# Optimization experiments

Measured on AMD Instinct MI355X. Metric: run time of the kernel, lower is better.

The kernel has to match this reference:

```python
import jax, jax.numpy as jnp
import numpy as np

N_NODES = 100000
NEG_SLOPE = 0.2  # PyG GATConv default


def gat_conv(x, src, dst, W, a_src, a_dst, n_nodes):
    """One PyG-style GATConv (with self-loops already appended to src/dst).
    x: [N, Fin], W: [Fin, H*C], a_src/a_dst: [H, C]. Returns [N, H, C]."""
    H, C = a_src.shape
    h = (x @ W).reshape(-1, H, C)                      # [N, H, C]
    s_src = jnp.einsum('nhc,hc->nh', h, a_src)         # [N, H]
    s_dst = jnp.einsum('nhc,hc->nh', h, a_dst)         # [N, H]
    e = jax.nn.leaky_relu(s_src[src] + s_dst[dst], NEG_SLOPE)  # [E, H]
    # segment softmax over incoming edges of each destination node
    e_max = jax.ops.segment_max(e, dst, num_segments=n_nodes)  # [N, H]
    e_exp = jnp.exp(e - e_max[dst])
    denom = jax.ops.segment_sum(e_exp, dst, num_segments=n_nodes)
    alpha = e_exp / (denom[dst] + 1e-16)               # [E, H]
    msg = h[src] * alpha[:, :, None]                   # [E, H, C]
    return jax.ops.segment_sum(msg, dst, num_segments=n_nodes)  # [N, H, C]


def setup_inputs() -> dict:
    key = jax.random.key(0)
    ks = jax.random.split(key, 10)
    in_dim, hidden, heads, out_dim = 128, 32, 4, 32
    N, E = N_NODES, 1600000
    x = jax.random.normal(ks[0], (N, in_dim), dtype=jnp.float32)
    edge_index = jax.random.randint(ks[1], (2, E), 0, N, dtype=jnp.int64)
    s = 0.1
    return {
        'x': x,
        'edge_index': edge_index,
        'W1': s * jax.random.normal(ks[2], (in_dim, heads * hidden), dtype=jnp.float32),
        'a_src1': s * jax.random.normal(ks[3], (heads, hidden), dtype=jnp.float32),
        'a_dst1': s * jax.random.normal(ks[4], (heads, hidden), dtype=jnp.float32),
        'b1': jnp.zeros((heads * hidden,), dtype=jnp.float32),
        'W2': s * jax.random.normal(ks[5], (heads * hidden, out_dim), dtype=jnp.float32),
        'a_src2': s * jax.random.normal(ks[6], (1, out_dim), dtype=jnp.float32),
        'a_dst2': s * jax.random.normal(ks[7], (1, out_dim), dtype=jnp.float32),
        'b2': jnp.zeros((out_dim,), dtype=jnp.float32),
    }


def reference(x, edge_index, W1, a_src1, a_dst1, b1, W2, a_src2, a_dst2, b2):
    N = x.shape[0]
    loops = jnp.arange(N, dtype=edge_index.dtype)
    src = jnp.concatenate([edge_index[0], loops])  # PyG adds self-loops
    dst = jnp.concatenate([edge_index[1], loops])
    h1 = gat_conv(x, src, dst, W1, a_src1, a_dst1, N)      # [N, H, C]
    h1 = jax.nn.elu(h1.reshape(N, -1) + b1)                # concat heads + bias, elu
    h2 = gat_conv(h1, src, dst, W2, a_src2, a_dst2, N)     # [N, 1, out]
    return h2.mean(axis=1) + b2                            # concat=False -> mean over heads
```

## Files before the change

### kernel.cpp

```cpp
#include <hip/hip_runtime.h>
#include <hip/hip_bf16.h>

#define NEG 0.2f
#define BK_SHIFT 9
#define BK_CAP 9216

typedef short short8 __attribute__((ext_vector_type(8)));
typedef float f32x4 __attribute__((ext_vector_type(4)));

__device__ __forceinline__ float lrelu(float x){ return x > 0.f ? x : NEG * x; }
__device__ __forceinline__ float elu_f(float x){ return x > 0.f ? x : expm1f(x); }
__device__ __forceinline__ unsigned short f2bf(float f){
  unsigned int u = __float_as_uint(f);
  unsigned int r = u + 0x7fffu + ((u >> 16) & 1u);
  return (unsigned short)(r >> 16);
}
__device__ __forceinline__ float bf2f(unsigned short u){
  return __uint_as_float(((unsigned int)u) << 16);
}
__device__ __forceinline__ float2 bfu2(unsigned int v){
  float2 r;
  r.x = __uint_as_float(v << 16);
  r.y = __uint_as_float(v & 0xffff0000u);
  return r;
}

__global__ __launch_bounds__(512) void k_binA_packW(
    const int* __restrict__ src, const int* __restrict__ dst, int E,
    int* __restrict__ gcursor, int2* __restrict__ ebuf,
    const float* __restrict__ W, unsigned short* __restrict__ Wp, int nA){
  __shared__ int hist[256];
  __shared__ int base[256];
  int t = threadIdx.x;
  int bid = blockIdx.x;
  if (bid >= nA){
    int idx = (bid - nA) * 512 + t;
    int n = idx >> 7, k = idx & 127;
    Wp[n * 128 + k] = f2bf(W[(size_t)k * 128 + n]);
    return;
  }
  if (t < 256) hist[t] = 0;
  __syncthreads();
  int e0 = bid * 4096;
  for (int j = 0; j < 8; j++){
    int e = e0 + j * 512 + t;
    if (e < E) atomicAdd(&hist[dst[e] >> BK_SHIFT], 1);
  }
  __syncthreads();
  if (t < 256){
    int cnt = hist[t];
    if (cnt > 0) base[t] = atomicAdd(&gcursor[t], cnt);
    hist[t] = 0;
  }
  __syncthreads();
  for (int j = 0; j < 8; j++){
    int e = e0 + j * 512 + t;
    if (e < E){
      int d = dst[e]; int b = d >> BK_SHIFT;
      int loc = atomicAdd(&hist[b], 1);
      ebuf[(size_t)b * BK_CAP + base[b] + loc] = make_int2(src[e], d);
    }
  }
}

__global__ __launch_bounds__(256, 3) void k_csrC_gemm1(
    const int2* __restrict__ ebuf, const int* __restrict__ gcount,
    int* __restrict__ rowp, int* __restrict__ csr, int N, int NBK, int total,
    const float* __restrict__ x, const unsigned short* __restrict__ Wp,
    const float* __restrict__ a_src, const float* __restrict__ a_dst,
    unsigned short* __restrict__ h_bf, float* __restrict__ ss, float* __restrict__ sd){
  __shared__ __align__(16) unsigned short Wt[128 * 136];
  __shared__ __align__(16) unsigned short Xb[64 * 136];
  int t = threadIdx.x;

  if (blockIdx.x < (unsigned)NBK){
    int* hist = (int*)Wt;
    int* psum = hist + 512;
    int* bsum = psum + 256;
    int b = blockIdx.x;
    int nbase = b << BK_SHIFT;
    int cnt = gcount[b];
    const int2* eb = ebuf + (size_t)b * BK_CAP;
    hist[t] = 0; hist[t + 256] = 0;
    int bv = 0;
    {
      int nodes = 0;
      if (t < NBK){ int nb = N - (t << BK_SHIFT); nodes = nb > 512 ? 512 : nb; bv = gcount[t] + nodes; }
      bsum[t] = bv;
    }
    __syncthreads();
    for (int off = 1; off < 256; off <<= 1){
      int xv = (t >= off) ? bsum[t - off] : 0;
      __syncthreads();
      bsum[t] += xv;
      __syncthreads();
    }
    for (int i = t; i < cnt; i += 256)
      atomicAdd(&hist[eb[i].y - nbase], 1);
    __syncthreads();
    int v0 = hist[2 * t], v1 = hist[2 * t + 1];
    int ps = v0 + v1;
    psum[t] = ps;
    __syncthreads();
    for (int off = 1; off < 256; off <<= 1){
      int xv = (t >= off) ? psum[t - off] : 0;
      __syncthreads();
      psum[t] += xv;
      __syncthreads();
    }
    {
      int eo = psum[t] - ps;
      int bb = (b == 0) ? 0 : bsum[b - 1];
      int n0 = 2 * t, n1 = 2 * t + 1;
      int r0 = bb + eo + n0;
      int r1 = bb + eo + v0 + n1;
      if (nbase + n0 < N) rowp[nbase + n0] = r0;
      if (nbase + n1 < N) rowp[nbase + n1] = r1;
      hist[n0] = r0; hist[n1] = r1;
    }
    if (b == 0 && t == 0) rowp[N] = total;
    __syncthreads();
    for (int i = t; i < cnt; i += 256){
      int2 e = eb[i];
      int pos = atomicAdd(&hist[e.y - nbase], 1);
      csr[pos] = e.x;
    }
    __syncthreads();
    {
      int n0 = 2 * t, n1 = 2 * t + 1;
      if (nbase + n0 < N) csr[hist[n0]] = nbase + n0;
      if (nbase + n1 < N) csr[hist[n1]] = nbase + n1;
    }
    return;
  }

  int rb = (blockIdx.x - NBK) * 64;

  #pragma unroll
  for (int j = 0; j < 8; j++){
    int fi = j * 256 + t;
    int n = fi >> 4, ch = fi & 15;
    *(uint4*)&Wt[n * 136 + ch * 8] = *(const uint4*)&Wp[n * 128 + ch * 8];
  }
  #pragma unroll
  for (int j = 0; j < 8; j++){
    int fi = j * 256 + t;
    int row = fi >> 5, k4 = (fi & 31) * 4;
    int gr = rb + row;
    float4 v = make_float4(0.f, 0.f, 0.f, 0.f);
    if (gr < N) v = *(const float4*)&x[(size_t)gr * 128 + k4];
    uint2 pk;
    pk.x = ((unsigned)f2bf(v.y) << 16) | f2bf(v.x);
    pk.y = ((unsigned)f2bf(v.w) << 16) | f2bf(v.z);
    *(uint2*)&Xb[row * 136 + k4] = pk;
  }
  __syncthreads();

  int w = t >> 6, l = t & 63;
  int m = l & 15, quad = l >> 4;
  f32x4 acc[8];
  #pragma unroll
  for (int ct = 0; ct < 8; ct++) acc[ct] = (f32x4){0.f, 0.f, 0.f, 0.f};

  #pragma unroll
  for (int kc = 0; kc < 4; kc++){
    short8 a = *(const short8*)&Xb[(w * 16 + m) * 136 + kc * 32 + quad * 8];
    #pragma unroll
    for (int ct = 0; ct < 8; ct++){
      short8 bfr = *(const short8*)&Wt[(ct * 16 + m) * 136 + kc * 32 + quad * 8];
      acc[ct] = __builtin_amdgcn_mfma_f32_16x16x32_bf16(a, bfr, acc[ct], 0, 0, 0);
    }
  }

  float as[8], ad[8];
  #pragma unroll
  for (int ct = 0; ct < 8; ct++){ as[ct] = a_src[ct * 16 + m]; ad[ct] = a_dst[ct * 16 + m]; }

  #pragma unroll
  for (int reg = 0; reg < 4; reg++){
    int gr = rb + w * 16 + quad * 4 + reg;
    bool ok = gr < N;
    if (ok){
      #pragma unroll
      for (int ct = 0; ct < 8; ct++)
        h_bf[(size_t)gr * 128 + ct * 16 + m] = f2bf(acc[ct][reg]);
    }
    #pragma unroll
    for (int hh = 0; hh < 4; hh++){
      float pss = acc[2*hh][reg] * as[2*hh] + acc[2*hh+1][reg] * as[2*hh+1];
      float pd = acc[2*hh][reg] * ad[2*hh] + acc[2*hh+1][reg] * ad[2*hh+1];
      pss += __shfl_xor(pss, 1, 16); pss += __shfl_xor(pss, 2, 16);
      pss += __shfl_xor(pss, 4, 16); pss += __shfl_xor(pss, 8, 16);
      pd += __shfl_xor(pd, 1, 16); pd += __shfl_xor(pd, 2, 16);
      pd += __shfl_xor(pd, 4, 16); pd += __shfl_xor(pd, 8, 16);
      if (m == 0 && ok){ ss[(size_t)gr * 4 + hh] = pss; sd[(size_t)gr * 4 + hh] = pd; }
    }
  }
}

__global__ __launch_bounds__(256) void k_agg1(
    const int* __restrict__ row_ptr, const int* __restrict__ csr_src,
    const float* __restrict__ ss, const float* __restrict__ sdst,
    const unsigned short* __restrict__ hb,
    unsigned int* __restrict__ out1_bf, int N){
  int n = blockIdx.x * 4 + (threadIdx.x >> 6);
  if (n >= N) return;
  int l = threadIdx.x & 63;
  int q  = (l & 7) + ((l >> 5) << 3);
  int hh = (l >> 3) & 3;
  int slot = l >> 4;
  int c = l & 15;
  int hd = c >> 2;
  float sdw = sdst[(size_t)n * 4 + hh];
  int beg = row_ptr[n], end = row_ptr[n + 1];

  float acc[8] = {0.f,0.f,0.f,0.f,0.f,0.f,0.f,0.f};
  float swacc = 0.f;

  int e = beg;
  int remaining = end - beg;
  int qc = q < remaining ? q : 0;
  int sj = __builtin_nontemporal_load(&csr_src[e + qc]);
  float sv = ss[(size_t)sj * 4 + hh];

  while (remaining > 0){
    int cur = remaining > 16 ? 16 : remaining;
    float wv = (q < cur) ? __expf(lrelu(sv + sdw)) : 0.f;
    swacc += wv;
    int sjc = sj;
    int rn = remaining - 16;
    if (rn > 0){
      int qn = q < rn ? q : 0;
      sj = __builtin_nontemporal_load(&csr_src[e + 16 + qn]);
      sv = ss[(size_t)sj * 4 + hh];
    }
    #pragma unroll
    for (int p = 0; p < 4; p++){
      if ((p << 2) < cur){
        int sl = ((p & 1) << 2) + slot + ((p >> 1) << 5);
        int s  = __shfl(sjc, sl, 64);
        float w = __shfl(wv, sl + (hd << 3), 64);
        uint4 u = *(const uint4*)&hb[(size_t)s * 128 + (c << 3)];
        float2 f0 = bfu2(u.x), f1 = bfu2(u.y), f2 = bfu2(u.z), f3 = bfu2(u.w);
        acc[0] += w * f0.x; acc[1] += w * f0.y;
        acc[2] += w * f1.x; acc[3] += w * f1.y;
        acc[4] += w * f2.x; acc[5] += w * f2.y;
        acc[6] += w * f3.x; acc[7] += w * f3.y;
      }
    }
    e += 16; remaining = rn;
  }

  #pragma unroll
  for (int i = 0; i < 8; i++){
    acc[i] += __shfl_xor(acc[i], 16, 64);
    acc[i] += __shfl_xor(acc[i], 32, 64);
  }
  swacc += __shfl_xor(swacc, 1, 64);
  swacc += __shfl_xor(swacc, 2, 64);
  swacc += __shfl_xor(swacc, 4, 64);
  swacc += __shfl_xor(swacc, 32, 64);
  float sw = __shfl(swacc, hd << 3, 64);
  float inv = 1.f / (sw + 1e-16f);
  if (slot == 0){
    unsigned int o0 = ((unsigned)f2bf(acc[1] * inv) << 16) | f2bf(acc[0] * inv);
    unsigned int o1 = ((unsigned)f2bf(acc[3] * inv) << 16) | f2bf(acc[2] * inv);
    unsigned int o2 = ((unsigned)f2bf(acc[5] * inv) << 16) | f2bf(acc[4] * inv);
    unsigned int o3 = ((unsigned)f2bf(acc[7] * inv) << 16) | f2bf(acc[6] * inv);
    uint4 o; o.x = o0; o.y = o1; o.z = o2; o.w = o3;
    *(uint4*)&out1_bf[(size_t)n * 64 + (c << 2)] = o;
  }
}

__global__ __launch_bounds__(256) void k_gemm2(
    const unsigned int* __restrict__ out1_bf, const float* __restrict__ b1,
    const float* __restrict__ W2,
    const float* __restrict__ a_src, const float* __restrict__ a_dst,
    unsigned short* __restrict__ h2_bf, float* __restrict__ s_src2, float* __restrict__ s_dst2, int N){
  __shared__ __align__(16) float Wl[128 * 32];
  __shared__ __align__(16) float Xl[64 * 132];
  int t = threadIdx.x;
  int rb = blockIdx.x * 64;

  const float4* Wg4 = (const float4*)W2;
  float4* Wl4 = (float4*)Wl;
  #pragma unroll
  for (int j = 0; j < 4; j++) Wl4[j * 256 + t] = Wg4[j * 256 + t];

  #pragma unroll
  for (int j = 0; j < 4; j++){
    int fi = j * 256 + t;
    int row = fi >> 4, q = fi & 15;
    int gr = rb + row;
    float v[8] = {0.f,0.f,0.f,0.f,0.f,0.f,0.f,0.f};
    if (gr < N){
      uint4 u = *(const uint4*)&out1_bf[(size_t)gr * 64 + q * 4];
      float4 bva = *(const float4*)&b1[q * 8];
      float4 bvb = *(const float4*)&b1[q * 8 + 4];
      v[0] = elu_f(bf2f((unsigned short)(u.x & 0xffff)) + bva.x);
      v[1] = elu_f(bf2f((unsigned short)(u.x >> 16))    + bva.y);
      v[2] = elu_f(bf2f((unsigned short)(u.y & 0xffff)) + bva.z);
      v[3] = elu_f(bf2f((unsigned short)(u.y >> 16))    + bva.w);
      v[4] = elu_f(bf2f((unsigned short)(u.z & 0xffff)) + bvb.x);
      v[5] = elu_f(bf2f((unsigned short)(u.z >> 16))    + bvb.y);
      v[6] = elu_f(bf2f((unsigned short)(u.w & 0xffff)) + bvb.z);
      v[7] = elu_f(bf2f((unsigned short)(u.w >> 16))    + bvb.w);
    }
    #pragma unroll
    for (int i = 0; i < 8; i++) Xl[row * 132 + q * 8 + i] = v[i];
  }
  __syncthreads();

  int cg = t & 7, rg = t >> 3;
  int c0 = cg * 4, r0 = rg * 2;
  float acc[2][4] = {};

  #pragma unroll 8
  for (int k = 0; k < 128; k++){
    float a0 = Xl[r0 * 132 + k];
    float a1 = Xl[(r0 + 1) * 132 + k];
    float4 b = *(float4*)&Wl[k * 32 + c0];
    acc[0][0] += a0 * b.x; acc[0][1] += a0 * b.y; acc[0][2] += a0 * b.z; acc[0][3] += a0 * b.w;
    acc[1][0] += a1 * b.x; acc[1][1] += a1 * b.y; acc[1][2] += a1 * b.z; acc[1][3] += a1 * b.w;
  }

  float as[4], ad[4];
  #pragma unroll
  for (int j = 0; j < 4; j++){ as[j] = a_src[c0 + j]; ad[j] = a_dst[c0 + j]; }
  #pragma unroll
  for (int i = 0; i < 2; i++){
    int row = rb + r0 + i;
    if (row < N){
      ushort4 o;
      o.x = f2bf(acc[i][0]); o.y = f2bf(acc[i][1]); o.z = f2bf(acc[i][2]); o.w = f2bf(acc[i][3]);
      *(ushort4*)&h2_bf[(size_t)row * 32 + c0] = o;
    }
    float ps = 0.f, pd = 0.f;
    #pragma unroll
    for (int j = 0; j < 4; j++){ ps += acc[i][j] * as[j]; pd += acc[i][j] * ad[j]; }
    ps += __shfl_xor(ps, 1, 8); ps += __shfl_xor(ps, 2, 8); ps += __shfl_xor(ps, 4, 8);
    pd += __shfl_xor(pd, 1, 8); pd += __shfl_xor(pd, 2, 8); pd += __shfl_xor(pd, 4, 8);
    if ((t & 7) == 0 && row < N){ s_src2[row] = ps; s_dst2[row] = pd; }
  }
}

__global__ __launch_bounds__(256) void k_agg2(
    const int* __restrict__ row_ptr, const int* __restrict__ csr_src,
    const float* __restrict__ ss2, const float* __restrict__ sd2,
    const unsigned short* __restrict__ h2bf, const float* __restrict__ b2,
    float* __restrict__ out, int N){
  int n = blockIdx.x * 4 + (threadIdx.x >> 6);
  if (n >= N) return;
  int l = threadIdx.x & 63;
  int q = l & 15;
  int slot = l >> 2;
  int ch4 = l & 3;
  float sdv = sd2[n];
  int beg = row_ptr[n], end = row_ptr[n + 1];

  float acc[8] = {0.f,0.f,0.f,0.f,0.f,0.f,0.f,0.f};
  float swacc = 0.f;

  int e = beg;
  int remaining = end - beg;
  int qc = q < remaining ? q : 0;
  int sj = __builtin_nontemporal_load(&csr_src[e + qc]);
  float sv = ss2[sj];

  while (remaining > 0){
    int cur = remaining > 16 ? 16 : remaining;
    float wv = (q < cur) ? __expf(lrelu(sv + sdv)) : 0.f;
    swacc += wv;
    int sjc = sj; float wvc = wv;
    int rn = remaining - 16;
    if (rn > 0){
      int qn = q < rn ? q : 0;
      sj = __builtin_nontemporal_load(&csr_src[e + 16 + qn]);
      sv = ss2[sj];
    }
    {
      int s  = __shfl(sjc, slot, 64);
      float w = __shfl(wvc, slot, 64);
      uint4 u = *(const uint4*)&h2bf[(size_t)s * 32 + (ch4 << 3)];
      float2 f0 = bfu2(u.x), f1 = bfu2(u.y), f2 = bfu2(u.z), f3 = bfu2(u.w);
      acc[0] += w * f0.x; acc[1] += w * f0.y;
      acc[2] += w * f1.x; acc[3] += w * f1.y;
      acc[4] += w * f2.x; acc[5] += w * f2.y;
      acc[6] += w * f3.x; acc[7] += w * f3.y;
    }
    e += 16; remaining = rn;
  }

  #pragma unroll
  for (int i = 0; i < 8; i++){
    acc[i] += __shfl_xor(acc[i], 4, 64);
    acc[i] += __shfl_xor(acc[i], 8, 64);
    acc[i] += __shfl_xor(acc[i], 16, 64);
    acc[i] += __shfl_xor(acc[i], 32, 64);
  }
  swacc += __shfl_xor(swacc, 1, 64);
  swacc += __shfl_xor(swacc, 2, 64);
  swacc += __shfl_xor(swacc, 4, 64);
  swacc += __shfl_xor(swacc, 8, 64);
  float inv = 1.f / (swacc + 1e-16f);
  if (slot == 0){
    float4 bva = *(const float4*)&b2[(ch4 << 3)];
    float4 bvb = *(const float4*)&b2[(ch4 << 3) + 4];
    float4 oa, ob;
    oa.x = acc[0] * inv + bva.x; oa.y = acc[1] * inv + bva.y;
    oa.z = acc[2] * inv + bva.z; oa.w = acc[3] * inv + bva.w;
    ob.x = acc[4] * inv + bvb.x; ob.y = acc[5] * inv + bvb.y;
    ob.z = acc[6] * inv + bvb.z; ob.w = acc[7] * inv + bvb.w;
    *(float4*)&out[(size_t)n * 32 + (ch4 << 3)] = oa;
    *(float4*)&out[(size_t)n * 32 + (ch4 << 3) + 4] = ob;
  }
}

extern "C" void kernel_launch(void* const* d_in, const int* in_sizes, int n_in,
                              void* d_out, int out_size, void* d_ws, size_t ws_size,
                              hipStream_t stream) {
  const float* x      = (const float*)d_in[0];
  const int*   ei     = (const int*)  d_in[1];
  const float* W1     = (const float*)d_in[2];
  const float* a_src1 = (const float*)d_in[3];
  const float* a_dst1 = (const float*)d_in[4];
  const float* b1     = (const float*)d_in[5];
  const float* W2     = (const float*)d_in[6];
  const float* a_src2 = (const float*)d_in[7];
  const float* a_dst2 = (const float*)d_in[8];
  const float* b2     = (const float*)d_in[9];
  float* out = (float*)d_out;

  int N = in_sizes[0] / 128;
  int E = in_sizes[1] / 2;
  const int* srcp = ei;
  const int* dstp = ei + E;
  int total = E + N;
  int NBK = (N + 511) >> 9;

  char* p = (char*)d_ws;
  auto alloc = [&](size_t bytes) -> void* {
    void* r = (void*)p; p += (bytes + 255) & ~(size_t)255; return r;
  };
  unsigned short* h_bf    = (unsigned short*)alloc((size_t)N * 128 * 2);
  unsigned int*   out1_bf = (unsigned int*)alloc((size_t)N * 64 * 4);
  unsigned short* h2_bf   = (unsigned short*)alloc((size_t)N * 32 * 2);
  unsigned short* Wp      = (unsigned short*)alloc(128 * 128 * 2);
  float* ss1  = (float*)alloc((size_t)N * 4 * 4);
  float* sd1  = (float*)alloc((size_t)N * 4 * 4);
  float* ss2  = (float*)alloc((size_t)N * 4);
  float* sd2  = (float*)alloc((size_t)N * 4);
  int* rowp   = (int*)alloc((size_t)(N + 1) * 4);
  int* csr    = (int*)alloc((size_t)total * 4);
  int* gcur   = (int*)alloc(256 * 4);
  int2* ebuf  = (int2*)out1_bf;
  (void)ws_size; (void)n_in; (void)out_size;

  int nA = (E + 4095) / 4096;
  int nG = (N + 63) / 64;

  hipMemsetAsync(gcur, 0, 256 * 4, stream);
  k_binA_packW<<<nA + 32, 512, 0, stream>>>(srcp, dstp, E, gcur, ebuf, W1, Wp, nA);
  k_csrC_gemm1<<<NBK + nG, 256, 0, stream>>>(ebuf, gcur, rowp, csr, N, NBK, total,
                                             x, Wp, a_src1, a_dst1, h_bf, ss1, sd1);
  k_agg1<<<(N + 3) / 4, 256, 0, stream>>>(rowp, csr, ss1, sd1, h_bf, out1_bf, N);
  k_gemm2<<<nG, 256, 0, stream>>>(out1_bf, b1, W2, a_src2, a_dst2, h2_bf, ss2, sd2, N);
  k_agg2<<<(N + 3) / 4, 256, 0, stream>>>(rowp, csr, ss2, sd2, h2_bf, b2, out, N);
}
```

Before: 313.6 us.

## Pack binned edges into 32-bit words and skip padded-lane gathers

The binned edge buffer now stores each edge as one 32-bit word, with the source index in the low 23 bits and the local destination offset in the high 9 bits. This halves the traffic of the scatter write and the CSR build reads. In both aggregation kernels, lanes whose edge slot lies beyond the current chunk no longer issue the feature-row gather, which removes wasted memory loads for low-degree tails. The csr index loads also drop the nontemporal hint. The packing assumes node ids fit in 23 bits, which holds for the given N.

```diff
diff --git a/kernel.cpp b/kernel.cpp
--- a/kernel.cpp
+++ b/kernel.cpp
@@ -25,9 +25,11 @@
   return r;
 }
 
+#define EB_SRC_MASK 0x7fffffu
+
 __global__ __launch_bounds__(512) void k_binA_packW(
     const int* __restrict__ src, const int* __restrict__ dst, int E,
-    int* __restrict__ gcursor, int2* __restrict__ ebuf,
+    int* __restrict__ gcursor, unsigned int* __restrict__ ebuf,
     const float* __restrict__ W, unsigned short* __restrict__ Wp, int nA){
   __shared__ int hist[256];
   __shared__ int base[256];
@@ -58,13 +60,14 @@
     if (e < E){
       int d = dst[e]; int b = d >> BK_SHIFT;
       int loc = atomicAdd(&hist[b], 1);
-      ebuf[(size_t)b * BK_CAP + base[b] + loc] = make_int2(src[e], d);
+      unsigned int dloc = (unsigned int)(d & ((1 << BK_SHIFT) - 1));
+      ebuf[(size_t)b * BK_CAP + base[b] + loc] = (unsigned int)src[e] | (dloc << 23);
     }
   }
 }
 
 __global__ __launch_bounds__(256, 3) void k_csrC_gemm1(
-    const int2* __restrict__ ebuf, const int* __restrict__ gcount,
+    const unsigned int* __restrict__ ebuf, const int* __restrict__ gcount,
     int* __restrict__ rowp, int* __restrict__ csr, int N, int NBK, int total,
     const float* __restrict__ x, const unsigned short* __restrict__ Wp,
     const float* __restrict__ a_src, const float* __restrict__ a_dst,
@@ -80,7 +83,7 @@
     int b = blockIdx.x;
     int nbase = b << BK_SHIFT;
     int cnt = gcount[b];
-    const int2* eb = ebuf + (size_t)b * BK_CAP;
+    const unsigned int* eb = ebuf + (size_t)b * BK_CAP;
     hist[t] = 0; hist[t + 256] = 0;
     int bv = 0;
     {
@@ -96,7 +99,7 @@
       __syncthreads();
     }
     for (int i = t; i < cnt; i += 256)
-      atomicAdd(&hist[eb[i].y - nbase], 1);
+      atomicAdd(&hist[eb[i] >> 23], 1);
     __syncthreads();
     int v0 = hist[2 * t], v1 = hist[2 * t + 1];
     int ps = v0 + v1;
@@ -121,9 +124,9 @@
     if (b == 0 && t == 0) rowp[N] = total;
     __syncthreads();
     for (int i = t; i < cnt; i += 256){
-      int2 e = eb[i];
-      int pos = atomicAdd(&hist[e.y - nbase], 1);
-      csr[pos] = e.x;
+      unsigned int e = eb[i];
+      int pos = atomicAdd(&hist[e >> 23], 1);
+      csr[pos] = (int)(e & EB_SRC_MASK);
     }
     __syncthreads();
     {
@@ -220,7 +223,7 @@
   int e = beg;
   int remaining = end - beg;
   int qc = q < remaining ? q : 0;
-  int sj = __builtin_nontemporal_load(&csr_src[e + qc]);
+  int sj = csr_src[e + qc];
   float sv = ss[(size_t)sj * 4 + hh];
 
   while (remaining > 0){
@@ -231,21 +234,24 @@
     int rn = remaining - 16;
     if (rn > 0){
       int qn = q < rn ? q : 0;
-      sj = __builtin_nontemporal_load(&csr_src[e + 16 + qn]);
+      sj = csr_src[e + 16 + qn];
       sv = ss[(size_t)sj * 4 + hh];
     }
     #pragma unroll
     for (int p = 0; p < 4; p++){
-      if ((p << 2) < cur){
+      int base_p = ((p & 1) << 2) + ((p >> 1) << 3);
+      if (base_p < cur){
         int sl = ((p & 1) << 2) + slot + ((p >> 1) << 5);
         int s  = __shfl(sjc, sl, 64);
         float w = __shfl(wv, sl + (hd << 3), 64);
-        uint4 u = *(const uint4*)&hb[(size_t)s * 128 + (c << 3)];
-        float2 f0 = bfu2(u.x), f1 = bfu2(u.y), f2 = bfu2(u.z), f3 = bfu2(u.w);
-        acc[0] += w * f0.x; acc[1] += w * f0.y;
-        acc[2] += w * f1.x; acc[3] += w * f1.y;
-        acc[4] += w * f2.x; acc[5] += w * f2.y;
-        acc[6] += w * f3.x; acc[7] += w * f3.y;
+        if (base_p + slot < cur){
+          uint4 u = *(const uint4*)&hb[(size_t)s * 128 + (c << 3)];
+          float2 f0 = bfu2(u.x), f1 = bfu2(u.y), f2 = bfu2(u.z), f3 = bfu2(u.w);
+          acc[0] += w * f0.x; acc[1] += w * f0.y;
+          acc[2] += w * f1.x; acc[3] += w * f1.y;
+          acc[4] += w * f2.x; acc[5] += w * f2.y;
+          acc[6] += w * f3.x; acc[7] += w * f3.y;
+        }
       }
     }
     e += 16; remaining = rn;
@@ -364,7 +370,7 @@
   int e = beg;
   int remaining = end - beg;
   int qc = q < remaining ? q : 0;
-  int sj = __builtin_nontemporal_load(&csr_src[e + qc]);
+  int sj = csr_src[e + qc];
   float sv = ss2[sj];
 
   while (remaining > 0){
@@ -375,18 +381,20 @@
     int rn = remaining - 16;
     if (rn > 0){
       int qn = q < rn ? q : 0;
-      sj = __builtin_nontemporal_load(&csr_src[e + 16 + qn]);
+      sj = csr_src[e + 16 + qn];
       sv = ss2[sj];
     }
     {
       int s  = __shfl(sjc, slot, 64);
       float w = __shfl(wvc, slot, 64);
-      uint4 u = *(const uint4*)&h2bf[(size_t)s * 32 + (ch4 << 3)];
-      float2 f0 = bfu2(u.x), f1 = bfu2(u.y), f2 = bfu2(u.z), f3 = bfu2(u.w);
-      acc[0] += w * f0.x; acc[1] += w * f0.y;
-      acc[2] += w * f1.x; acc[3] += w * f1.y;
-      acc[4] += w * f2.x; acc[5] += w * f2.y;
-      acc[6] += w * f3.x; acc[7] += w * f3.y;
+      if (slot < cur){
+        uint4 u = *(const uint4*)&h2bf[(size_t)s * 32 + (ch4 << 3)];
+        float2 f0 = bfu2(u.x), f1 = bfu2(u.y), f2 = bfu2(u.z), f3 = bfu2(u.w);
+        acc[0] += w * f0.x; acc[1] += w * f0.y;
+        acc[2] += w * f1.x; acc[3] += w * f1.y;
+        acc[4] += w * f2.x; acc[5] += w * f2.y;
+        acc[6] += w * f3.x; acc[7] += w * f3.y;
+      }
     }
     e += 16; remaining = rn;
   }
@@ -453,7 +461,7 @@
   int* rowp   = (int*)alloc((size_t)(N + 1) * 4);
   int* csr    = (int*)alloc((size_t)total * 4);
   int* gcur   = (int*)alloc(256 * 4);
-  int2* ebuf  = (int2*)out1_bf;
+  unsigned int* ebuf = (unsigned int*)out1_bf;
   (void)ws_size; (void)n_in; (void)out_size;
 
   int nA = (E + 4095) / 4096;
```

New measurement: 309.1 us. Within noise of the previous version (-1.4%).
